# Kernel tuning notes

Hardware: AMD Instinct MI355X
Metric: run time of the kernel (lower is better)

Reference implementation:

```python
import jax, jax.numpy as jnp
import numpy as np


def hilbert_perm(M: int) -> np.ndarray:
    """Permutation ordering the first M cells of a Hilbert curve on a 2^k x 2^k grid."""
    side = 1
    while side * side < M:
        side *= 2
    idx = np.arange(M)
    x = (idx % side).astype(np.int64)
    y = (idx // side).astype(np.int64)
    d = np.zeros(M, dtype=np.int64)
    s = side // 2
    while s > 0:
        rx = ((x & s) > 0).astype(np.int64)
        ry = ((y & s) > 0).astype(np.int64)
        d += s * s * ((3 * rx) ^ ry)
        swap = ry == 0
        flip = swap & (rx == 1)
        x2 = np.where(flip, s - 1 - x, x)
        y2 = np.where(flip, s - 1 - y, y)
        x, y = np.where(swap, y2, x2), np.where(swap, x2, y2)
        s //= 2
    return np.argsort(d, kind='stable')


SEGMENT_SIZE = 512


def setup_inputs() -> dict:
    key = jax.random.key(0)
    ks = jax.random.split(key, 5)
    B, M, H, D = 2, 8192, 8, 64
    hd = H * D  # 512
    q = jax.random.normal(ks[0], (B, M, H, D), dtype=jnp.float32)
    k = jax.random.normal(ks[1], (B, M, H, D), dtype=jnp.float32)
    v = jax.random.normal(ks[2], (B, M, H, D), dtype=jnp.float32)
    w_qkv = jax.random.normal(ks[3], (3 * hd, hd), dtype=jnp.float32) * (hd ** -0.5)
    w_out = jax.random.normal(ks[4], (hd, hd), dtype=jnp.float32) * (hd ** -0.5)
    return {"q": q, "k": k, "v": v, "w_qkv": w_qkv, "w_out": w_out}


def reference(q, k, v, w_qkv, w_out):
    B, M, H, D = q.shape
    hd = H * D
    S = SEGMENT_SIZE
    n_seg = M // S
    # Wrapper: mean over heads, then channel-repeat to hidden_dim
    x = q.mean(axis=2)                       # [B, M, D]
    x = jnp.tile(x, (1, 1, H))               # [B, M, hd]
    # HilbertAttentionCore: fused QKV projection
    qkv = jnp.einsum('bmc,fc->bmf', x, w_qkv)  # [B, M, 3*hd]
    qh, kh, vh = jnp.split(qkv, 3, axis=-1)
    # Hilbert-curve reordering (static permutation of seq dim)
    perm = jnp.asarray(hilbert_perm(M))
    inv = jnp.argsort(perm)
    def seg(t):
        t = t[:, perm]                       # reorder seq
        return t.reshape(B, n_seg, S, H, D)
    qs, ks_, vs = seg(qh), seg(kh), seg(vh)
    scale = D ** -0.5
    scores = jnp.einsum('bnshd,bnthd->bnhst', qs, ks_) * scale  # [B,n_seg,H,S,S]
    attn = jax.nn.softmax(scores, axis=-1)
    out = jnp.einsum('bnhst,bnthd->bnshd', attn, vs)            # [B,n_seg,S,H,D]
    out = out.reshape(B, M, hd)[:, inv]      # undo Hilbert ordering
    out = jnp.einsum('bmc,fc->bmf', out, w_out)  # output projection
    return out.reshape(B, M, H, D)
```

## Files before the change

### kernel.cpp

```cpp
#include <hip/hip_runtime.h>


typedef short bfrag __attribute__((ext_vector_type(8)));
typedef float ffrag __attribute__((ext_vector_type(4)));
typedef short svec4 __attribute__((ext_vector_type(4)));
typedef unsigned uvec4 __attribute__((ext_vector_type(4)));

__device__ inline short f2bf(float x) {
  unsigned u = __builtin_bit_cast(unsigned, x);
  u = (u + 0x7fffu + ((u >> 16) & 1u)) >> 16;
  return (short)u;
}
__device__ inline float fexp2(float x) {
#if __has_builtin(__builtin_amdgcn_exp2f)
  return __builtin_amdgcn_exp2f(x);
#else
  return __expf(x * 0.6931471805599453f);
#endif
}
__device__ inline unsigned cvtpk(float a, float b) {
  unsigned r;
  asm("v_cvt_pk_bf16_f32 %0, %1, %2" : "=v"(r) : "v"(a), "v"(b));
  return r;
}
__device__ inline void gload_lds16(const void* g, void* l) {
  __builtin_amdgcn_global_load_lds(
      (const __attribute__((address_space(1))) unsigned*)g,
      (__attribute__((address_space(3))) unsigned*)l, 16, 0, 0);
}

__device__ inline int d2xy128(int d) {
  int x = 0, y = 0, t = d;
  for (int s = 1; s < 128; s <<= 1) {
    int rx = 1 & (t >> 1);
    int ry = 1 & (t ^ rx);
    if (ry == 0) {
      if (rx == 1) { x = s - 1 - x; y = s - 1 - y; }
      int tt = x; x = y; y = tt;
    }
    x += s * rx;
    y += s * ry;
    t >>= 2;
  }
  return y * 128 + x;
}

__global__ __launch_bounds__(256) void prep_kernel(
    const float* __restrict__ q, const float* __restrict__ w_qkv,
    const float* __restrict__ w_out, short* __restrict__ xmean,
    short* __restrict__ weff, short* __restrict__ woutb,
    int* __restrict__ perm) {
  int i = blockIdx.x * 256 + threadIdx.x;
  if (i < 1048576) {
    int bm = i >> 6, d = i & 63;
    const float* p = q + (size_t)bm * 512 + d;
    float s = 0.f;
#pragma unroll
    for (int h = 0; h < 8; ++h) s += p[h * 64];
    xmean[i] = f2bf(s * 0.125f);
  } else if (i < 1048576 + 98304) {
    int j = i - 1048576;
    int f = j >> 6;
    const float* p = w_qkv + (size_t)f * 512 + (j & 63);
    float s = 0.f;
#pragma unroll
    for (int r = 0; r < 8; ++r) s += p[r * 64];
    if (f < 512) s *= 0.125f * 1.44269504088896f;
    weff[j] = f2bf(s);
  } else if (i < 1048576 + 98304 + 262144) {
    int j = i - 1048576 - 98304;
    woutb[j] = f2bf(w_out[j]);
  } else if (i < 1048576 + 98304 + 262144 + 8192) {
    int r = i - (1048576 + 98304 + 262144);
    perm[r] = d2xy128(r < 4096 ? r : r + 8192);
  }
}

__global__ __launch_bounds__(256, 2) void qkv_kernel(
    const short* __restrict__ xmean, const short* __restrict__ weff,
    const int* __restrict__ perm, short* __restrict__ Qs,
    short* __restrict__ Ks, short* __restrict__ Vt) {
  __shared__ short Wlds[384 * 64];
  __shared__ short Sb[4][2][16 * 72];
  int tid = threadIdx.x;
  int w = tid >> 6, lane = tid & 63;
  int ml = lane & 15, quad = lane >> 4;
  int rg = blockIdx.x >> 2, fq = blockIdx.x & 3;
  int r0 = rg * 64 + w * 16;
  int r = r0 + ml;
  int b = r >> 13, p = r & 8191;
  int src = (b << 13) + perm[p];
  bfrag a0 = *(const bfrag*)(xmean + (size_t)src * 64 + quad * 8);
  bfrag a1 = *(const bfrag*)(xmean + (size_t)src * 64 + 32 + quad * 8);
  int p0 = r0 & 8191;
  int bq = r0 >> 13;
  int nseg = p0 >> 9;
  int sbase = (p0 & 511) + quad * 4;

  {
    int lrow = lane >> 3;
    int lu = lane & 7;
    const short* wsrc = weff + (size_t)(fq * 384 + w * 96 + lrow) * 64 +
                        ((lu ^ (lrow & 7)) * 8);
#pragma unroll
    for (int i = 0; i < 12; ++i)
      gload_lds16(wsrc + (size_t)i * 8 * 64,
                  (char*)Wlds + w * 12288 + i * 1024);
  }
  __syncthreads();

#pragma unroll 1
  for (int gg = 0; gg < 6; ++gg) {
    int nt0 = fq * 24 + gg * 4;
    int f0g = nt0 * 16;
    short* sb = &Sb[w][gg & 1][0];
    if (f0g < 1024) {
#pragma unroll
      for (int t = 0; t < 4; ++t) {
        int row = (gg * 4 + t) * 16 + ml;
        const char* Wb = (const char*)Wlds + row * 128;
        int sw = (row & 7) << 4;
        bfrag wf0 = *(const bfrag*)(Wb + ((quad << 4) ^ sw));
        bfrag wf1 = *(const bfrag*)(Wb + (((4 + quad) << 4) ^ sw));
        ffrag acc = {0.f, 0.f, 0.f, 0.f};
        acc = __builtin_amdgcn_mfma_f32_16x16x32_bf16(wf0, a0, acc, 0, 0, 0);
        acc = __builtin_amdgcn_mfma_f32_16x16x32_bf16(wf1, a1, acc, 0, 0, 0);
        svec4 pk;
#pragma unroll
        for (int g = 0; g < 4; ++g) pk[g] = f2bf(acc[g]);
        *(svec4*)((char*)sb + ml * 144 + t * 32 + quad * 8) = pk;
      }
      __builtin_amdgcn_sched_barrier(0);
      int rrow = lane >> 3;
      int cu = lane & 7;
      bfrag v0 = *(const bfrag*)((char*)sb + rrow * 144 + cu * 16);
      bfrag v1 = *(const bfrag*)((char*)sb + (rrow + 8) * 144 + cu * 16);
      short* dst = (f0g < 512) ? Qs : Ks;
      int fo = f0g & 511;
      *(bfrag*)(dst + (size_t)(r0 + rrow) * 512 + fo + cu * 8) = v0;
      *(bfrag*)(dst + (size_t)(r0 + rrow + 8) * 512 + fo + cu * 8) = v1;
    } else {
#pragma unroll
      for (int t = 0; t < 4; ++t) {
        int nt = nt0 + t;
        int row = (gg * 4 + t) * 16 + ml;
        const char* Wb = (const char*)Wlds + row * 128;
        int sw = (row & 7) << 4;
        bfrag wf0 = *(const bfrag*)(Wb + ((quad << 4) ^ sw));
        bfrag wf1 = *(const bfrag*)(Wb + (((4 + quad) << 4) ^ sw));
        ffrag acc = {0.f, 0.f, 0.f, 0.f};
        acc = __builtin_amdgcn_mfma_f32_16x16x32_bf16(a0, wf0, acc, 0, 0, 0);
        acc = __builtin_amdgcn_mfma_f32_16x16x32_bf16(a1, wf1, acc, 0, 0, 0);
        int fl = nt * 16 + ml - 1024;
        int hh = fl >> 6, dd = fl & 63;
        svec4 pk;
#pragma unroll
        for (int g = 0; g < 4; ++g) pk[g] = f2bf(acc[g]);
        *(svec4*)(Vt + ((((size_t)bq * 16 + nseg) * 8 + hh) * 64 + dd) * 512 +
                  sbase) = pk;
      }
    }
  }
}

__global__ __launch_bounds__(256, 2) void attn_kernel(
    const short* __restrict__ Qs, const short* __restrict__ Ks,
    const short* __restrict__ Vt, const int* __restrict__ perm,
    short* __restrict__ aout) {
  __shared__ short Klds[2][64 * 64];
  __shared__ short Vlds[2][64 * 64];
  int tid = threadIdx.x;
  int w = tid >> 6, lane = tid & 63;
  int ml = lane & 15, quad = lane >> 4;
  int sh = blockIdx.x & 255;
  int qq = blockIdx.x >> 8;
  int b = sh >> 7;
  int n = (sh >> 3) & 15;
  int h = sh & 7;
  size_t segrow = (size_t)(b * 8192 + n * 512);
  const short* Qseg = Qs + segrow * 512 + h * 64;
  const short* Kseg = Ks + segrow * 512 + h * 64;
  const short* Vseg = Vt + (((size_t)(b * 16 + n) * 8 + h) * 64) * 512;
  int q0 = qq * 256 + w * 64;
  bfrag qa[4][2];
#pragma unroll
  for (int nq = 0; nq < 4; ++nq)
#pragma unroll
    for (int ks = 0; ks < 2; ++ks)
      qa[nq][ks] = *(const bfrag*)(Qseg + (size_t)(q0 + nq * 16 + ml) * 512 +
                                   ks * 32 + quad * 8);
  ffrag o[4][4];
  float lrun[4] = {0.f, 0.f, 0.f, 0.f};
#pragma unroll
  for (int nq = 0; nq < 4; ++nq)
#pragma unroll
    for (int dt = 0; dt < 4; ++dt) o[nq][dt] = (ffrag){0.f, 0.f, 0.f, 0.f};

  int srow = lane >> 3;
  int sug = (lane & 7) ^ srow;

  auto stage = [&](int buf, int t0) {
    char* Kd = (char*)&Klds[buf][0] + w * 2048;
    char* Vd = (char*)&Vlds[buf][0] + w * 2048;
    gload_lds16(Kseg + (size_t)(t0 + w * 16 + srow) * 512 + sug * 8, Kd);
    gload_lds16(Kseg + (size_t)(t0 + w * 16 + 8 + srow) * 512 + sug * 8,
                Kd + 1024);
    gload_lds16(Vseg + (size_t)(w * 16 + srow) * 512 + t0 + sug * 8, Vd);
    gload_lds16(Vseg + (size_t)(w * 16 + 8 + srow) * 512 + t0 + sug * 8,
                Vd + 1024);
  };

  auto body = [&](int buf) {
    const char* Kb = (const char*)&Klds[buf][0];
    const char* Vb = (const char*)&Vlds[buf][0];
#pragma unroll
    for (int s = 0; s < 2; ++s) {
      bfrag kk[2][2], vv[4];
#pragma unroll
      for (int mt = 0; mt < 2; ++mt)
#pragma unroll
        for (int ks = 0; ks < 2; ++ks) {
          int row = s * 32 + mt * 16 + ml;
          int byte = row * 128 + ks * 64 + quad * 16;
          kk[mt][ks] = *(const bfrag*)(Kb + (byte ^ ((row & 7) << 4)));
        }
#pragma unroll
      for (int dt = 0; dt < 4; ++dt) {
        int row = dt * 16 + ml;
        int byte = row * 128 + s * 64 + quad * 16;
        vv[dt] = *(const bfrag*)(Vb + (byte ^ ((row & 7) << 4)));
      }
#pragma unroll
      for (int nq = 0; nq < 4; ++nq) {
        ffrag c0 = {0.f, 0.f, 0.f, 0.f}, c1 = {0.f, 0.f, 0.f, 0.f};
        c0 = __builtin_amdgcn_mfma_f32_16x16x32_bf16(kk[0][0], qa[nq][0], c0, 0, 0, 0);
        c0 = __builtin_amdgcn_mfma_f32_16x16x32_bf16(kk[0][1], qa[nq][1], c0, 0, 0, 0);
        c1 = __builtin_amdgcn_mfma_f32_16x16x32_bf16(kk[1][0], qa[nq][0], c1, 0, 0, 0);
        c1 = __builtin_amdgcn_mfma_f32_16x16x32_bf16(kk[1][1], qa[nq][1], c1, 0, 0, 0);
        float e0 = fexp2(c0[0]), e1 = fexp2(c0[1]);
        float e2 = fexp2(c0[2]), e3 = fexp2(c0[3]);
        float e4 = fexp2(c1[0]), e5 = fexp2(c1[1]);
        float e6 = fexp2(c1[2]), e7 = fexp2(c1[3]);
        lrun[nq] += ((e0 + e1) + (e2 + e3)) + ((e4 + e5) + (e6 + e7));
        unsigned A0 = cvtpk(e0, e1), A1 = cvtpk(e2, e3);
        unsigned A2 = cvtpk(e4, e5), A3 = cvtpk(e6, e7);
        asm("v_permlane32_swap_b32 %0, %1" : "+v"(A0), "+v"(A2));
        asm("v_permlane16_swap_b32 %0, %1" : "+v"(A0), "+v"(A2));
        asm("v_permlane32_swap_b32 %0, %1" : "+v"(A1), "+v"(A3));
        asm("v_permlane16_swap_b32 %0, %1" : "+v"(A1), "+v"(A3));
        uvec4 pu;
        pu[0] = A0;
        pu[1] = A1;
        pu[2] = A2;
        pu[3] = A3;
        bfrag pa = __builtin_bit_cast(bfrag, pu);
#pragma unroll
        for (int dt = 0; dt < 4; ++dt)
          o[nq][dt] = __builtin_amdgcn_mfma_f32_16x16x32_bf16(vv[dt], pa,
                                                              o[nq][dt], 0, 0, 0);
      }
    }
  };

  stage(0, 0);
  __syncthreads();
  int cur = 0;
#pragma unroll 1
  for (int jj = 0; jj < 7; ++jj) {
    stage(cur ^ 1, (jj + 1) * 64);
    body(cur);
    __syncthreads();
    cur ^= 1;
  }
  body(cur);

#pragma unroll
  for (int nq = 0; nq < 4; ++nq) {
    float l = lrun[nq];
    l += __shfl_xor(l, 16);
    l += __shfl_xor(l, 32);
    float inv = 1.f / l;
    int sout = q0 + nq * 16 + ml;
    int om = perm[n * 512 + sout];
    size_t base = ((size_t)(b * 8192 + om)) * 512 + h * 64;
#pragma unroll
    for (int dt = 0; dt < 4; ++dt) {
      svec4 pk;
#pragma unroll
      for (int g = 0; g < 4; ++g) pk[g] = f2bf(o[nq][dt][g] * inv);
      *(svec4*)(aout + base + dt * 16 + quad * 4) = pk;
    }
  }
}

__global__ __launch_bounds__(256, 2) void proj_kernel(
    const short* __restrict__ aout, const short* __restrict__ woutb,
    float* __restrict__ out) {
  __shared__ short As[2][128 * 64];
  __shared__ short Bs[2][128 * 64];
  int tid = threadIdx.x;
  int w = tid >> 6, lane = tid & 63;
  int ml = lane & 15, quad = lane >> 4;
  int rb = blockIdx.x & 127;
  int cb = blockIdx.x >> 7;
  int r0 = rb * 128, c0 = cb * 128;
  int wr = (w >> 1) * 64, wc = (w & 1) * 64;

  ffrag acc[4][4];
#pragma unroll
  for (int m = 0; m < 4; ++m)
#pragma unroll
    for (int n = 0; n < 4; ++n) acc[m][n] = (ffrag){0.f, 0.f, 0.f, 0.f};

  int srow = w * 32 + (lane >> 3);
  int scol = (lane & 7) * 8;
  const short* gA = aout + (size_t)(r0 + srow) * 512 + scol;
  const short* gB = woutb + (size_t)(c0 + srow) * 512 + scol;

  auto stage = [&](int buf, int k0) {
#pragma unroll
    for (int i = 0; i < 4; ++i) {
      gload_lds16(gA + (size_t)i * 8 * 512 + k0,
                  (char*)&As[buf][0] + w * 4096 + i * 1024);
      gload_lds16(gB + (size_t)i * 8 * 512 + k0,
                  (char*)&Bs[buf][0] + w * 4096 + i * 1024);
    }
  };
  auto compute = [&](int buf) {
#pragma unroll
    for (int kk = 0; kk < 2; ++kk) {
      bfrag af[4], bf[4];
#pragma unroll
      for (int m = 0; m < 4; ++m)
        af[m] = *(const bfrag*)&As[buf][(wr + m * 16 + ml) * 64 + kk * 32 +
                                        quad * 8];
#pragma unroll
      for (int n = 0; n < 4; ++n)
        bf[n] = *(const bfrag*)&Bs[buf][(wc + n * 16 + ml) * 64 + kk * 32 +
                                        quad * 8];
#pragma unroll
      for (int m = 0; m < 4; ++m)
#pragma unroll
        for (int n = 0; n < 4; ++n)
          acc[m][n] = __builtin_amdgcn_mfma_f32_16x16x32_bf16(bf[n], af[m],
                                                              acc[m][n], 0, 0, 0);
    }
  };

  stage(0, 0);
  __syncthreads();
  int cur = 0;
#pragma unroll 1
  for (int t = 0; t < 7; ++t) {
    stage(cur ^ 1, (t + 1) * 64);
    compute(cur);
    __syncthreads();
    cur ^= 1;
  }
  compute(cur);

#pragma unroll
  for (int m = 0; m < 4; ++m)
#pragma unroll
    for (int n = 0; n < 4; ++n)
      *(ffrag*)(out + (size_t)(r0 + wr + m * 16 + ml) * 512 + c0 + wc +
                n * 16 + quad * 4) = acc[m][n];
}

extern "C" void kernel_launch(void* const* d_in, const int* in_sizes, int n_in,
                              void* d_out, int out_size, void* d_ws,
                              size_t ws_size, hipStream_t stream) {
  const float* q = (const float*)d_in[0];
  const float* w_qkv = (const float*)d_in[3];
  const float* w_out = (const float*)d_in[4];
  float* out = (float*)d_out;

  char* ws = (char*)d_ws;
  int* perm = (int*)ws;
  short* xmean = (short*)(ws + 32768);
  short* weff = (short*)(ws + 2129920);
  short* woutb = (short*)(ws + 2326528);
  short* Qs = (short*)(ws + 2850816);
  short* Ks = (short*)(ws + 19628032);
  short* Vt = (short*)(ws + 36405248);
  short* aout = (short*)(ws + 53182464);

  prep_kernel<<<5536, 256, 0, stream>>>(q, w_qkv, w_out, xmean, weff, woutb,
                                        perm);
  qkv_kernel<<<1024, 256, 0, stream>>>(xmean, weff, perm, Qs, Ks, Vt);
  attn_kernel<<<512, 256, 0, stream>>>(Qs, Ks, Vt, perm, aout);
  proj_kernel<<<512, 256, 0, stream>>>(aout, woutb, out);
}
```

Before: 183.8 us.

## Prefetch two stages ahead with partial vmcnt waits and raw barriers

```diff
diff --git a/kernel.cpp b/kernel.cpp
--- a/kernel.cpp
+++ b/kernel.cpp
@@ -263,16 +263,20 @@
   };
 
   stage(0, 0);
-  __syncthreads();
-  int cur = 0;
+  stage(1, 64);
 #pragma unroll 1
   for (int jj = 0; jj < 7; ++jj) {
-    stage(cur ^ 1, (jj + 1) * 64);
-    body(cur);
-    __syncthreads();
-    cur ^= 1;
-  }
-  body(cur);
+    asm volatile("s_waitcnt vmcnt(4)" ::: "memory");
+    __builtin_amdgcn_s_barrier();
+    body(jj & 1);
+    if (jj < 6) {
+      __builtin_amdgcn_s_barrier();
+      stage(jj & 1, (jj + 2) * 64);
+    }
+  }
+  asm volatile("s_waitcnt vmcnt(0)" ::: "memory");
+  __builtin_amdgcn_s_barrier();
+  body(1);
 
 #pragma unroll
   for (int nq = 0; nq < 4; ++nq) {
@@ -348,16 +352,20 @@
   };
 
   stage(0, 0);
-  __syncthreads();
-  int cur = 0;
+  stage(1, 64);
 #pragma unroll 1
   for (int t = 0; t < 7; ++t) {
-    stage(cur ^ 1, (t + 1) * 64);
-    compute(cur);
-    __syncthreads();
-    cur ^= 1;
-  }
-  compute(cur);
+    asm volatile("s_waitcnt vmcnt(8)" ::: "memory");
+    __builtin_amdgcn_s_barrier();
+    compute(t & 1);
+    if (t < 6) {
+      __builtin_amdgcn_s_barrier();
+      stage(t & 1, (t + 2) * 64);
+    }
+  }
+  asm volatile("s_waitcnt vmcnt(0)" ::: "memory");
+  __builtin_amdgcn_s_barrier();
+  compute(1);
 
 #pragma unroll
   for (int m = 0; m < 4; ++m)
```

Result: no change. 183.3 us (-0.3%).
